# Performance work log

Measured on AMD Instinct MI355X. Metric: run time of the kernel, lower is better.

The kernel has to match this reference:

```python
import jax, jax.numpy as jnp
import numpy as np

N_HEAD = 16
EMBED = 1024
HEAD_DIM = EMBED // N_HEAD  # 64
HALF = HEAD_DIM // 2        # 32
T = 2048                    # total packed tokens
NSEG = 4
SEG = T // NSEG             # 512 tokens per packed sequence
SCALE = HEAD_DIM ** -0.5


def _apply_rotary_vision(t, freqs):
    # t: [T, H, D], freqs: [T, D/2] -> Qwen2-VL style vision RoPE
    cos = jnp.concatenate([jnp.cos(freqs), jnp.cos(freqs)], axis=-1)[:, None, :]  # [T,1,D]
    sin = jnp.concatenate([jnp.sin(freqs), jnp.sin(freqs)], axis=-1)[:, None, :]
    t1, t2 = t[..., :HALF], t[..., HALF:]
    rot = jnp.concatenate([-t2, t1], axis=-1)  # rotate_half
    return t * cos + rot * sin


def setup_inputs() -> dict:
    key = jax.random.key(0)
    k1, k2, k3, k4, k5 = jax.random.split(key, 5)
    hidden_states = jax.random.normal(k1, (T, EMBED), dtype=jnp.float32)
    cu_seqlens = (jnp.arange(NSEG + 1, dtype=jnp.int32) * SEG)  # [0,512,...,2048]
    # realistic rotary freqs: position within each segment * inverse frequencies
    pos = jnp.tile(jnp.arange(SEG, dtype=jnp.float32), NSEG)  # [T]
    inv_freq = 1.0 / (10000.0 ** (jnp.arange(HALF, dtype=jnp.float32) / HALF))
    rotary_pos_emb = pos[:, None] * inv_freq[None, :]  # [T, HALF]
    std = 0.02
    wq = jax.random.normal(k2, (EMBED, EMBED), dtype=jnp.float32) * std
    wk = jax.random.normal(k3, (EMBED, EMBED), dtype=jnp.float32) * std
    wv = jax.random.normal(k4, (EMBED, EMBED), dtype=jnp.float32) * std
    wo = jax.random.normal(k5, (EMBED, EMBED), dtype=jnp.float32) * std
    return {"hidden_states": hidden_states, "cu_seqlens": cu_seqlens,
            "rotary_pos_emb": rotary_pos_emb, "wq": wq, "wk": wk, "wv": wv, "wo": wo}


def reference(hidden_states, cu_seqlens, rotary_pos_emb, wq, wk, wv, wo):
    # QKV projections (nn.Linear, bias=False): y = x @ W.T
    q = (hidden_states @ wq.T).reshape(T, N_HEAD, HEAD_DIM)
    k = (hidden_states @ wk.T).reshape(T, N_HEAD, HEAD_DIM)
    v = (hidden_states @ wv.T).reshape(T, N_HEAD, HEAD_DIM)
    q = _apply_rotary_vision(q, rotary_pos_emb)
    k = _apply_rotary_vision(k, rotary_pos_emb)
    # varlen (block-diagonal, non-causal) attention over packed segments
    seg_id = jnp.searchsorted(cu_seqlens, jnp.arange(T, dtype=cu_seqlens.dtype), side='right')
    same_seg = seg_id[:, None] == seg_id[None, :]  # [T, T]
    scores = jnp.einsum('thd,shd->hts', q, k) * SCALE  # [H, T, T]
    scores = jnp.where(same_seg[None, :, :], scores, jnp.finfo(scores.dtype).min)
    probs = jax.nn.softmax(scores, axis=-1)
    attn = jnp.einsum('hts,shd->thd', probs, v).reshape(T, EMBED)
    return attn @ wo.T
```

## Files before the change

### kernel.cpp

```cpp
#include <hip/hip_runtime.h>
#include <cstdint>

#define T_TOK 2048
#define EMBED 1024
#define NH    16
#define HD    64
#define HALF  32
#define SEG   512
#define SL    (0.125f * 1.44269504088896f)

typedef __attribute__((ext_vector_type(8))) __bf16 bf16x8;
typedef __attribute__((ext_vector_type(4))) float  f32x4;
typedef unsigned short u16;
typedef unsigned int   u32;

__device__ __forceinline__ u16 f2bf(float f) {
  u32 u = __builtin_bit_cast(u32, f);
  u += 0x7fffu + ((u >> 16) & 1u);
  return (u16)(u >> 16);
}

__device__ __forceinline__ void gld_lds16(const void* g, void* l) {
  __builtin_amdgcn_global_load_lds(
      reinterpret_cast<__attribute__((address_space(1))) u32*>(
          reinterpret_cast<uintptr_t>(g)),
      reinterpret_cast<__attribute__((address_space(3))) u32*>(
          reinterpret_cast<uintptr_t>(l)),
      16, 0, 0);
}

__global__ __launch_bounds__(256) void convert_k(
    const float* __restrict__ H,  const float* __restrict__ wq,
    const float* __restrict__ wk, const float* __restrict__ wv,
    const float* __restrict__ wo, u16* __restrict__ dst) {
  const size_t gid = (size_t)blockIdx.x * 256 + threadIdx.x;
  const size_t e = gid * 4;
  const float* src; size_t off;
  const size_t HN = (size_t)T_TOK * EMBED;
  if (e < HN) { src = H; off = e; }
  else {
    size_t r = e - HN;
    int w = (int)(r >> 20);
    off = r & ((1u << 20) - 1);
    src = (w == 0) ? wq : (w == 1) ? wk : (w == 2) ? wv : wo;
  }
  const float4 v = *(const float4*)(src + off);
  ushort4 o;
  o.x = f2bf(v.x); o.y = f2bf(v.y); o.z = f2bf(v.z); o.w = f2bf(v.w);
  *(ushort4*)(dst + e) = o;
}

__global__ __launch_bounds__(256) void qkv_k(
    const u16* __restrict__ Hb, const u16* __restrict__ Wb,
    const float* __restrict__ rope, u16* __restrict__ Qb,
    u16* __restrict__ Khh, u16* __restrict__ Vss) {
  constexpr int K = 1024, N = 1024;
  __shared__ alignas(16) u16 As[2][2][64 * 32];
  __shared__ alignas(16) u16 Bs[2][2][128 * 32];
  const int tid = threadIdx.x;
  const int wave = tid >> 6, lane = tid & 63;
  const int quad = lane >> 4, l16 = lane & 15;
  const int bm = blockIdx.y * 64, bn = blockIdx.x * 128;
  const int z = blockIdx.z;
  const u16* Bz = Wb + ((size_t)z << 20);
  const int wm = (wave >> 1) * 32, wn = (wave & 1) * 64;

  f32x4 acc[2][4];
#pragma unroll
  for (int i = 0; i < 2; ++i)
#pragma unroll
    for (int j = 0; j < 4; ++j) { f32x4 zz = {0.f, 0.f, 0.f, 0.f}; acc[i][j] = zz; }

  const int srow = tid >> 2, scol = (tid & 3) * 8;
  const u16* gA = Hb + (size_t)(bm + srow) * K + scol;
  const u16* gB = Bz + (size_t)(bn + srow) * K + scol;

#pragma unroll
  for (int p = 0; p < 2; ++p) {
    gld_lds16(gA + p * 32, (char*)&As[0][p][0] + wave * 1024);
    gld_lds16(gB + p * 32, (char*)&Bs[0][p][0] + wave * 1024);
    gld_lds16(gB + (size_t)64 * K + p * 32, (char*)&Bs[0][p][64 * 32] + wave * 1024);
  }

  for (int kk = 0; kk < K; kk += 64) {
    __syncthreads();
    const int cur = (kk >> 6) & 1, nxt = cur ^ 1;
    if (kk + 64 < K) {
      const int kn = kk + 64;
#pragma unroll
      for (int p = 0; p < 2; ++p) {
        gld_lds16(gA + kn + p * 32, (char*)&As[nxt][p][0] + wave * 1024);
        gld_lds16(gB + kn + p * 32, (char*)&Bs[nxt][p][0] + wave * 1024);
        gld_lds16(gB + (size_t)64 * K + kn + p * 32,
                  (char*)&Bs[nxt][p][64 * 32] + wave * 1024);
      }
    }
#pragma unroll
    for (int p = 0; p < 2; ++p) {
      const u16* Ac = &As[cur][p][0];
      const u16* Bc = &Bs[cur][p][0];
      bf16x8 af[2], bfv[4];
#pragma unroll
      for (int i = 0; i < 2; ++i)
        af[i] = *(const bf16x8*)(Ac + (wm + i * 16 + l16) * 32 + quad * 8);
#pragma unroll
      for (int j = 0; j < 4; ++j)
        bfv[j] = *(const bf16x8*)(Bc + (wn + j * 16 + l16) * 32 + quad * 8);
#pragma unroll
      for (int i = 0; i < 2; ++i)
#pragma unroll
        for (int j = 0; j < 4; ++j)
          acc[i][j] = __builtin_amdgcn_mfma_f32_16x16x32_bf16(af[i], bfv[j],
                                                              acc[i][j], 0, 0, 0);
    }
  }

  const int h = (bn + wn) >> 6;
  if (z == 0) {
#pragma unroll
    for (int i = 0; i < 2; ++i)
#pragma unroll
      for (int r = 0; r < 4; ++r) {
        const int t = bm + wm + i * 16 + quad * 4 + r;
        const float f0 = rope[t * HALF + l16];
        const float f1 = rope[t * HALF + 16 + l16];
        float s0, c0, s1, c1;
        __sincosf(f0, &s0, &c0);
        __sincosf(f1, &s1, &c1);
        const float v0 = acc[i][0][r], v1 = acc[i][1][r];
        const float v2 = acc[i][2][r], v3 = acc[i][3][r];
        const size_t base = (size_t)t * N + bn + wn + l16;
        Qb[base]      = f2bf(v0 * c0 - v2 * s0);
        Qb[base + 16] = f2bf(v1 * c1 - v3 * s1);
        Qb[base + 32] = f2bf(v2 * c0 + v0 * s0);
        Qb[base + 48] = f2bf(v3 * c1 + v1 * s1);
      }
  } else if (z == 1) {
#pragma unroll
    for (int i = 0; i < 2; ++i)
#pragma unroll
      for (int r = 0; r < 4; ++r) {
        const int t = bm + wm + i * 16 + quad * 4 + r;
        const float f0 = rope[t * HALF + l16];
        const float f1 = rope[t * HALF + 16 + l16];
        float s0, c0, s1, c1;
        __sincosf(f0, &s0, &c0);
        __sincosf(f1, &s1, &c1);
        const float v0 = acc[i][0][r], v1 = acc[i][1][r];
        const float v2 = acc[i][2][r], v3 = acc[i][3][r];
        const size_t b0 = ((size_t)(h * 2 + 0) * T_TOK + t) * 32;
        const size_t b1 = ((size_t)(h * 2 + 1) * T_TOK + t) * 32;
        Khh[b0 + l16]      = f2bf(v0 * c0 - v2 * s0);
        Khh[b0 + 16 + l16] = f2bf(v1 * c1 - v3 * s1);
        Khh[b1 + l16]      = f2bf(v2 * c0 + v0 * s0);
        Khh[b1 + 16 + l16] = f2bf(v3 * c1 + v1 * s1);
      }
  } else {
#pragma unroll
    for (int i = 0; i < 2; ++i) {
      const int t0 = bm + wm + i * 16 + quad * 4;
      const int tp = t0 >> 5, toff = t0 & 31;
#pragma unroll
      for (int j = 0; j < 4; ++j) {
        const int d = j * 16 + l16;
        ushort4 pk;
        pk.x = f2bf(acc[i][j][0]); pk.y = f2bf(acc[i][j][1]);
        pk.z = f2bf(acc[i][j][2]); pk.w = f2bf(acc[i][j][3]);
        *(ushort4*)(Vss + ((size_t)(h * 64 + tp) * 64 + d) * 32 + toff) = pk;
      }
    }
  }
}

__global__ __launch_bounds__(256) void attn_st(
    const u16* __restrict__ Qb, const u16* __restrict__ Khh,
    const u16* __restrict__ Vss, u16* __restrict__ Ab) {
  const int b = blockIdx.x;
  const int qt = b & 7, seg = (b >> 3) & 3, h = b >> 5;
  const int tid = threadIdx.x;
  const int wave = tid >> 6, lane = tid & 63;
  const int quad = lane >> 4, l16 = lane & 15;

  __shared__ alignas(16) u16 Ks[2][64 * 32];
  __shared__ alignas(16) u16 Vs[2][64 * 32];
  __shared__ alignas(16) u16 Pl[4][16 * 72];

  const int qbase = seg * SEG + qt * 64 + wave * 16;
  const u16* qp = Qb + (size_t)(qbase + l16) * EMBED + h * HD + quad * 8;
  const bf16x8 qf0 = *(const bf16x8*)qp;
  const bf16x8 qf1 = *(const bf16x8*)(qp + 32);

  const u16* Ksrc0 = Khh + ((size_t)(h * 2 + 0) * T_TOK + seg * SEG) * 32;
  const u16* Ksrc1 = Khh + ((size_t)(h * 2 + 1) * T_TOK + seg * SEG) * 32;
  const u16* Vsrc  = Vss + ((size_t)(h * 64 + seg * 16) * 64) * 32;

  float mold[4] = {-1e30f, -1e30f, -1e30f, -1e30f};
  float lsum[4] = {0.f, 0.f, 0.f, 0.f};
  f32x4 O[4];
#pragma unroll
  for (int nt = 0; nt < 4; ++nt) { f32x4 z = {0.f, 0.f, 0.f, 0.f}; O[nt] = z; }

  u16* pw = Pl[wave];
  const int toff = tid * 8;

  uint4 kreg0 = *(const uint4*)(Ksrc0 + toff);
  uint4 kreg1 = *(const uint4*)(Ksrc1 + toff);
  uint4 vreg0 = *(const uint4*)(Vsrc + toff);
  uint4 vreg1 = *(const uint4*)(Vsrc + 2048 + toff);

  for (int cc = 0; cc < 8; ++cc) {
    *(uint4*)((char*)&Ks[0][0] + tid * 16) = kreg0;
    *(uint4*)((char*)&Ks[1][0] + tid * 16) = kreg1;
    *(uint4*)((char*)&Vs[0][0] + tid * 16) = vreg0;
    *(uint4*)((char*)&Vs[1][0] + tid * 16) = vreg1;
    __syncthreads();
    if (cc + 1 < 8) {
      const size_t kc = (size_t)(cc + 1) * 2048 + toff;
      const size_t vc = (size_t)(cc + 1) * 4096 + toff;
      kreg0 = *(const uint4*)(Ksrc0 + kc);
      kreg1 = *(const uint4*)(Ksrc1 + kc);
      vreg0 = *(const uint4*)(Vsrc + vc);
      vreg1 = *(const uint4*)(Vsrc + vc + 2048);
    }
    f32x4 S[4];
#pragma unroll
    for (int kt = 0; kt < 4; ++kt) {
      const bf16x8 k0 = *(const bf16x8*)&Ks[0][(kt * 16 + l16) * 32 + quad * 8];
      const bf16x8 k1 = *(const bf16x8*)&Ks[1][(kt * 16 + l16) * 32 + quad * 8];
      f32x4 s = {0.f, 0.f, 0.f, 0.f};
      s = __builtin_amdgcn_mfma_f32_16x16x32_bf16(qf0, k0, s, 0, 0, 0);
      s = __builtin_amdgcn_mfma_f32_16x16x32_bf16(qf1, k1, s, 0, 0, 0);
      S[kt] = s;
    }
    bf16x8 vf0[4], vf1[4];
#pragma unroll
    for (int nt = 0; nt < 4; ++nt) {
      vf0[nt] = *(const bf16x8*)&Vs[0][(nt * 16 + l16) * 32 + quad * 8];
      vf1[nt] = *(const bf16x8*)&Vs[1][(nt * 16 + l16) * 32 + quad * 8];
    }
    float mx[4], al[4];
#pragma unroll
    for (int r = 0; r < 4; ++r) {
      float m = fmaxf(fmaxf(S[0][r], S[1][r]), fmaxf(S[2][r], S[3][r]));
#pragma unroll
      for (int off = 1; off < 16; off <<= 1) m = fmaxf(m, __shfl_xor(m, off));
      float mn = fmaxf(mold[r], m);
      al[r] = exp2f((mold[r] - mn) * SL);
      mold[r] = mn;
      mx[r] = mn;
    }
    float ps[4] = {0.f, 0.f, 0.f, 0.f};
#pragma unroll
    for (int kt = 0; kt < 4; ++kt)
#pragma unroll
      for (int r = 0; r < 4; ++r) {
        float p = exp2f((S[kt][r] - mx[r]) * SL);
        ps[r] += p;
        pw[(quad * 4 + r) * 72 + kt * 16 + l16] = f2bf(p);
      }
#pragma unroll
    for (int r = 0; r < 4; ++r) lsum[r] = lsum[r] * al[r] + ps[r];
#pragma unroll
    for (int nt = 0; nt < 4; ++nt) {
      O[nt][0] *= al[0]; O[nt][1] *= al[1];
      O[nt][2] *= al[2]; O[nt][3] *= al[3];
    }
    const u16* pp = pw + l16 * 72 + quad * 8;
    const bf16x8 pf0 = *(const bf16x8*)pp;
    const bf16x8 pf1 = *(const bf16x8*)(pp + 32);
#pragma unroll
    for (int nt = 0; nt < 4; ++nt) {
      O[nt] = __builtin_amdgcn_mfma_f32_16x16x32_bf16(pf0, vf0[nt], O[nt], 0, 0, 0);
      O[nt] = __builtin_amdgcn_mfma_f32_16x16x32_bf16(pf1, vf1[nt], O[nt], 0, 0, 0);
    }
    __syncthreads();
  }
#pragma unroll
  for (int r = 0; r < 4; ++r) {
    float l = lsum[r];
#pragma unroll
    for (int off = 1; off < 16; off <<= 1) l += __shfl_xor(l, off);
    lsum[r] = 1.f / l;
  }
#pragma unroll
  for (int nt = 0; nt < 4; ++nt)
#pragma unroll
    for (int r = 0; r < 4; ++r) {
      const int trow = qbase + quad * 4 + r;
      Ab[(size_t)trow * EMBED + h * HD + nt * 16 + l16] = f2bf(O[nt][r] * lsum[r]);
    }
}

__global__ __launch_bounds__(256) void oproj_k(
    const u16* __restrict__ Ab, const u16* __restrict__ Wo,
    float* __restrict__ out) {
  constexpr int K = 1024, N = 1024;
  __shared__ alignas(16) u16 As[2][2][64 * 32];
  __shared__ alignas(16) u16 Bs[2][2][64 * 32];
  const int tid = threadIdx.x;
  const int wave = tid >> 6, lane = tid & 63;
  const int quad = lane >> 4, l16 = lane & 15;
  const int bm = blockIdx.y * 64, bn = blockIdx.x * 64;

  f32x4 acc[4];
#pragma unroll
  for (int j = 0; j < 4; ++j) { f32x4 z = {0.f, 0.f, 0.f, 0.f}; acc[j] = z; }

  const int srow = tid >> 2, scol = (tid & 3) * 8;
  const u16* gA = Ab + (size_t)(bm + srow) * K + scol;
  const u16* gB = Wo + (size_t)(bn + srow) * K + scol;

#pragma unroll
  for (int p = 0; p < 2; ++p) {
    gld_lds16(gA + p * 32, (char*)&As[0][p][0] + wave * 1024);
    gld_lds16(gB + p * 32, (char*)&Bs[0][p][0] + wave * 1024);
  }

  for (int kk = 0; kk < K; kk += 64) {
    __syncthreads();
    const int cur = (kk >> 6) & 1, nxt = cur ^ 1;
    if (kk + 64 < K) {
      const int kn = kk + 64;
#pragma unroll
      for (int p = 0; p < 2; ++p) {
        gld_lds16(gA + kn + p * 32, (char*)&As[nxt][p][0] + wave * 1024);
        gld_lds16(gB + kn + p * 32, (char*)&Bs[nxt][p][0] + wave * 1024);
      }
    }
#pragma unroll
    for (int p = 0; p < 2; ++p) {
      const u16* Ac = &As[cur][p][0];
      const u16* Bc = &Bs[cur][p][0];
      const bf16x8 af = *(const bf16x8*)(Ac + (wave * 16 + l16) * 32 + quad * 8);
      bf16x8 bfv[4];
#pragma unroll
      for (int j = 0; j < 4; ++j)
        bfv[j] = *(const bf16x8*)(Bc + (j * 16 + l16) * 32 + quad * 8);
#pragma unroll
      for (int j = 0; j < 4; ++j)
        acc[j] = __builtin_amdgcn_mfma_f32_16x16x32_bf16(af, bfv[j],
                                                         acc[j], 0, 0, 0);
    }
  }

#pragma unroll
  for (int r = 0; r < 4; ++r) {
    const int row = bm + wave * 16 + quad * 4 + r;
#pragma unroll
    for (int j = 0; j < 4; ++j)
      out[(size_t)row * N + bn + j * 16 + l16] = acc[j][r];
  }
}

extern "C" void kernel_launch(void* const* d_in, const int* in_sizes, int n_in,
                              void* d_out, int out_size, void* d_ws,
                              size_t ws_size, hipStream_t stream) {
  const float* H    = (const float*)d_in[0];
  const float* rope = (const float*)d_in[2];
  const float* wq   = (const float*)d_in[3];
  const float* wk   = (const float*)d_in[4];
  const float* wv   = (const float*)d_in[5];
  const float* wo   = (const float*)d_in[6];
  float* out        = (float*)d_out;

  constexpr size_t M1 = (size_t)1 << 20;
  if (ws_size < 28 * M1) return;

  u16* ws16 = (u16*)d_ws;
  u16* Hb  = ws16;
  u16* Wb  = ws16 + 2 * M1;
  u16* Qb  = ws16 + 6 * M1;
  u16* Khh = ws16 + 8 * M1;
  u16* Vss = ws16 + 10 * M1;
  u16* Ab  = ws16 + 12 * M1;

  convert_k<<<6144, 256, 0, stream>>>(H, wq, wk, wv, wo, ws16);
  qkv_k<<<dim3(8, 32, 3), 256, 0, stream>>>(Hb, Wb, rope, Qb, Khh, Vss);
  attn_st<<<512, 256, 0, stream>>>(Qb, Khh, Vss, Ab);
  oproj_k<<<dim3(16, 32), 256, 0, stream>>>(Ab, Wb + 3 * M1, out);
}
```

Before: 131.6 us.

## Pre-pack GEMM operands into MFMA fragment layout and load directly to registers

The conversion kernel now writes hidden states and weights in a tiled layout where each 16x32 MFMA fragment is contiguous, and attention writes its output in the same packed layout. The QKV and output-projection GEMMs then drop LDS staging and barriers, reading fragments straight from global memory into registers with a two-stage register double buffer. This removes LDS traffic and __syncthreads, but gives up the sharing of tiles across waves that LDS provided, so each wave reloads operands from global/L2.

```diff
diff --git a/kernel.cpp b/kernel.cpp
--- a/kernel.cpp
+++ b/kernel.cpp
@@ -20,13 +20,9 @@
   return (u16)(u >> 16);
 }
 
-__device__ __forceinline__ void gld_lds16(const void* g, void* l) {
-  __builtin_amdgcn_global_load_lds(
-      reinterpret_cast<__attribute__((address_space(1))) u32*>(
-          reinterpret_cast<uintptr_t>(g)),
-      reinterpret_cast<__attribute__((address_space(3))) u32*>(
-          reinterpret_cast<uintptr_t>(l)),
-      16, 0, 0);
+__device__ __forceinline__ size_t pidx(int t, int k) {
+  return ((size_t)((t >> 4) * 32 + (k >> 5)) << 9) +
+         ((((k >> 3) & 3) * 16 + (t & 15)) << 3) + (k & 7);
 }
 
 __global__ __launch_bounds__(256) void convert_k(
@@ -34,36 +30,42 @@
     const float* __restrict__ wk, const float* __restrict__ wv,
     const float* __restrict__ wo, u16* __restrict__ dst) {
   const size_t gid = (size_t)blockIdx.x * 256 + threadIdx.x;
-  const size_t e = gid * 4;
-  const float* src; size_t off;
+  const size_t e8 = gid * 8;
+  const float* src; size_t off, base;
   const size_t HN = (size_t)T_TOK * EMBED;
-  if (e < HN) { src = H; off = e; }
+  if (e8 < HN) { src = H; off = e8; base = 0; }
   else {
-    size_t r = e - HN;
+    size_t r = e8 - HN;
     int w = (int)(r >> 20);
     off = r & ((1u << 20) - 1);
     src = (w == 0) ? wq : (w == 1) ? wk : (w == 2) ? wv : wo;
-  }
-  const float4 v = *(const float4*)(src + off);
-  ushort4 o;
-  o.x = f2bf(v.x); o.y = f2bf(v.y); o.z = f2bf(v.z); o.w = f2bf(v.w);
-  *(ushort4*)(dst + e) = o;
+    base = HN + ((size_t)w << 20);
+  }
+  const int t = (int)(off >> 10), k = (int)(off & 1023);
+  const float4 v0 = *(const float4*)(src + off);
+  const float4 v1 = *(const float4*)(src + off + 4);
+  ushort4 o0, o1;
+  o0.x = f2bf(v0.x); o0.y = f2bf(v0.y); o0.z = f2bf(v0.z); o0.w = f2bf(v0.w);
+  o1.x = f2bf(v1.x); o1.y = f2bf(v1.y); o1.z = f2bf(v1.z); o1.w = f2bf(v1.w);
+  u16* d = dst + base + pidx(t, k);
+  *(ushort4*)d = o0;
+  *(ushort4*)(d + 4) = o1;
 }
 
 __global__ __launch_bounds__(256) void qkv_k(
-    const u16* __restrict__ Hb, const u16* __restrict__ Wb,
+    const u16* __restrict__ Hp, const u16* __restrict__ Wp,
     const float* __restrict__ rope, u16* __restrict__ Qb,
     u16* __restrict__ Khh, u16* __restrict__ Vss) {
-  constexpr int K = 1024, N = 1024;
-  __shared__ alignas(16) u16 As[2][2][64 * 32];
-  __shared__ alignas(16) u16 Bs[2][2][128 * 32];
+  constexpr int N = 1024;
   const int tid = threadIdx.x;
   const int wave = tid >> 6, lane = tid & 63;
   const int quad = lane >> 4, l16 = lane & 15;
   const int bm = blockIdx.y * 64, bn = blockIdx.x * 128;
   const int z = blockIdx.z;
-  const u16* Bz = Wb + ((size_t)z << 20);
+  const u16* Bp = Wp + ((size_t)z << 20);
   const int wm = (wave >> 1) * 32, wn = (wave & 1) * 64;
+  const int t16 = (bm + wm) >> 4;
+  const int n16 = (bn + wn) >> 4;
 
   f32x4 acc[2][4];
 #pragma unroll
@@ -71,47 +73,48 @@
 #pragma unroll
     for (int j = 0; j < 4; ++j) { f32x4 zz = {0.f, 0.f, 0.f, 0.f}; acc[i][j] = zz; }
 
-  const int srow = tid >> 2, scol = (tid & 3) * 8;
-  const u16* gA = Hb + (size_t)(bm + srow) * K + scol;
-  const u16* gB = Bz + (size_t)(bn + srow) * K + scol;
-
-#pragma unroll
-  for (int p = 0; p < 2; ++p) {
-    gld_lds16(gA + p * 32, (char*)&As[0][p][0] + wave * 1024);
-    gld_lds16(gB + p * 32, (char*)&Bs[0][p][0] + wave * 1024);
-    gld_lds16(gB + (size_t)64 * K + p * 32, (char*)&Bs[0][p][64 * 32] + wave * 1024);
-  }
-
-  for (int kk = 0; kk < K; kk += 64) {
-    __syncthreads();
-    const int cur = (kk >> 6) & 1, nxt = cur ^ 1;
-    if (kk + 64 < K) {
-      const int kn = kk + 64;
-#pragma unroll
-      for (int p = 0; p < 2; ++p) {
-        gld_lds16(gA + kn + p * 32, (char*)&As[nxt][p][0] + wave * 1024);
-        gld_lds16(gB + kn + p * 32, (char*)&Bs[nxt][p][0] + wave * 1024);
-        gld_lds16(gB + (size_t)64 * K + kn + p * 32,
-                  (char*)&Bs[nxt][p][64 * 32] + wave * 1024);
-      }
-    }
-#pragma unroll
-    for (int p = 0; p < 2; ++p) {
-      const u16* Ac = &As[cur][p][0];
-      const u16* Bc = &Bs[cur][p][0];
-      bf16x8 af[2], bfv[4];
+  const u16* pa = Hp + ((size_t)t16 << 14) + lane * 8;
+  const u16* pb = Bp + ((size_t)n16 << 14) + lane * 8;
+
+  bf16x8 aF[2][2], bF[2][4];
+#pragma unroll
+  for (int s = 0; s < 2; ++s) {
+#pragma unroll
+    for (int i = 0; i < 2; ++i)
+      aF[s][i] = *(const bf16x8*)(pa + (((size_t)i * 32 + s) << 9));
+#pragma unroll
+    for (int j = 0; j < 4; ++j)
+      bF[s][j] = *(const bf16x8*)(pb + (((size_t)j * 32 + s) << 9));
+  }
+
+  for (int kp = 0; kp < 32; kp += 2) {
+#pragma unroll
+    for (int i = 0; i < 2; ++i)
+#pragma unroll
+      for (int j = 0; j < 4; ++j)
+        acc[i][j] = __builtin_amdgcn_mfma_f32_16x16x32_bf16(aF[0][i], bF[0][j],
+                                                            acc[i][j], 0, 0, 0);
+    if (kp + 2 < 32) {
 #pragma unroll
       for (int i = 0; i < 2; ++i)
-        af[i] = *(const bf16x8*)(Ac + (wm + i * 16 + l16) * 32 + quad * 8);
-#pragma unroll
-      for (int j = 0; j < 4; ++j)
-        bfv[j] = *(const bf16x8*)(Bc + (wn + j * 16 + l16) * 32 + quad * 8);
+        aF[0][i] = *(const bf16x8*)(pa + (((size_t)i * 32 + kp + 2) << 9));
+#pragma unroll
+      for (int j = 0; j < 4; ++j)
+        bF[0][j] = *(const bf16x8*)(pb + (((size_t)j * 32 + kp + 2) << 9));
+    }
+#pragma unroll
+    for (int i = 0; i < 2; ++i)
+#pragma unroll
+      for (int j = 0; j < 4; ++j)
+        acc[i][j] = __builtin_amdgcn_mfma_f32_16x16x32_bf16(aF[1][i], bF[1][j],
+                                                            acc[i][j], 0, 0, 0);
+    if (kp + 3 < 32) {
 #pragma unroll
       for (int i = 0; i < 2; ++i)
-#pragma unroll
-        for (int j = 0; j < 4; ++j)
-          acc[i][j] = __builtin_amdgcn_mfma_f32_16x16x32_bf16(af[i], bfv[j],
-                                                              acc[i][j], 0, 0, 0);
+        aF[1][i] = *(const bf16x8*)(pa + (((size_t)i * 32 + kp + 3) << 9));
+#pragma unroll
+      for (int j = 0; j < 4; ++j)
+        bF[1][j] = *(const bf16x8*)(pb + (((size_t)j * 32 + kp + 3) << 9));
     }
   }
 
@@ -174,7 +177,7 @@
 
 __global__ __launch_bounds__(256) void attn_st(
     const u16* __restrict__ Qb, const u16* __restrict__ Khh,
-    const u16* __restrict__ Vss, u16* __restrict__ Ab) {
+    const u16* __restrict__ Vss, u16* __restrict__ Abp) {
   const int b = blockIdx.x;
   const int qt = b & 7, seg = (b >> 3) & 3, h = b >> 5;
   const int tid = threadIdx.x;
@@ -282,64 +285,65 @@
     for (int off = 1; off < 16; off <<= 1) l += __shfl_xor(l, off);
     lsum[r] = 1.f / l;
   }
-#pragma unroll
-  for (int nt = 0; nt < 4; ++nt)
-#pragma unroll
-    for (int r = 0; r < 4; ++r) {
-      const int trow = qbase + quad * 4 + r;
-      Ab[(size_t)trow * EMBED + h * HD + nt * 16 + l16] = f2bf(O[nt][r] * lsum[r]);
-    }
+  const int t16 = qbase >> 4;
+#pragma unroll
+  for (int nt = 0; nt < 4; ++nt) {
+    const int kp = h * 2 + (nt >> 1);
+    const int k32q = (nt & 1) * 2 + (l16 >> 3);
+    u16* dst = Abp + (((size_t)t16 * 32 + kp) << 9) + (l16 & 7);
+#pragma unroll
+    for (int r = 0; r < 4; ++r)
+      dst[(size_t)(k32q * 16 + quad * 4 + r) << 3] = f2bf(O[nt][r] * lsum[r]);
+  }
 }
 
 __global__ __launch_bounds__(256) void oproj_k(
-    const u16* __restrict__ Ab, const u16* __restrict__ Wo,
+    const u16* __restrict__ Abp, const u16* __restrict__ Wop,
     float* __restrict__ out) {
-  constexpr int K = 1024, N = 1024;
-  __shared__ alignas(16) u16 As[2][2][64 * 32];
-  __shared__ alignas(16) u16 Bs[2][2][64 * 32];
+  constexpr int N = 1024;
   const int tid = threadIdx.x;
   const int wave = tid >> 6, lane = tid & 63;
   const int quad = lane >> 4, l16 = lane & 15;
   const int bm = blockIdx.y * 64, bn = blockIdx.x * 64;
+  const int t16 = (bm + wave * 16) >> 4;
+  const int n16 = bn >> 4;
 
   f32x4 acc[4];
 #pragma unroll
   for (int j = 0; j < 4; ++j) { f32x4 z = {0.f, 0.f, 0.f, 0.f}; acc[j] = z; }
 
-  const int srow = tid >> 2, scol = (tid & 3) * 8;
-  const u16* gA = Ab + (size_t)(bm + srow) * K + scol;
-  const u16* gB = Wo + (size_t)(bn + srow) * K + scol;
-
-#pragma unroll
-  for (int p = 0; p < 2; ++p) {
-    gld_lds16(gA + p * 32, (char*)&As[0][p][0] + wave * 1024);
-    gld_lds16(gB + p * 32, (char*)&Bs[0][p][0] + wave * 1024);
-  }
-
-  for (int kk = 0; kk < K; kk += 64) {
-    __syncthreads();
-    const int cur = (kk >> 6) & 1, nxt = cur ^ 1;
-    if (kk + 64 < K) {
-      const int kn = kk + 64;
-#pragma unroll
-      for (int p = 0; p < 2; ++p) {
-        gld_lds16(gA + kn + p * 32, (char*)&As[nxt][p][0] + wave * 1024);
-        gld_lds16(gB + kn + p * 32, (char*)&Bs[nxt][p][0] + wave * 1024);
-      }
-    }
-#pragma unroll
-    for (int p = 0; p < 2; ++p) {
-      const u16* Ac = &As[cur][p][0];
-      const u16* Bc = &Bs[cur][p][0];
-      const bf16x8 af = *(const bf16x8*)(Ac + (wave * 16 + l16) * 32 + quad * 8);
-      bf16x8 bfv[4];
-#pragma unroll
-      for (int j = 0; j < 4; ++j)
-        bfv[j] = *(const bf16x8*)(Bc + (j * 16 + l16) * 32 + quad * 8);
-#pragma unroll
-      for (int j = 0; j < 4; ++j)
-        acc[j] = __builtin_amdgcn_mfma_f32_16x16x32_bf16(af, bfv[j],
-                                                         acc[j], 0, 0, 0);
+  const u16* pa = Abp + ((size_t)t16 << 14) + lane * 8;
+  const u16* pb = Wop + ((size_t)n16 << 14) + lane * 8;
+
+  bf16x8 aF[2], bF[2][4];
+#pragma unroll
+  for (int s = 0; s < 2; ++s) {
+    aF[s] = *(const bf16x8*)(pa + ((size_t)s << 9));
+#pragma unroll
+    for (int j = 0; j < 4; ++j)
+      bF[s][j] = *(const bf16x8*)(pb + (((size_t)j * 32 + s) << 9));
+  }
+
+  for (int kp = 0; kp < 32; kp += 2) {
+#pragma unroll
+    for (int j = 0; j < 4; ++j)
+      acc[j] = __builtin_amdgcn_mfma_f32_16x16x32_bf16(aF[0], bF[0][j],
+                                                       acc[j], 0, 0, 0);
+    if (kp + 2 < 32) {
+      aF[0] = *(const bf16x8*)(pa + ((size_t)(kp + 2) << 9));
+#pragma unroll
+      for (int j = 0; j < 4; ++j)
+        bF[0][j] = *(const bf16x8*)(pb + (((size_t)j * 32 + kp + 2) << 9));
+    }
+#pragma unroll
+    for (int j = 0; j < 4; ++j)
+      acc[j] = __builtin_amdgcn_mfma_f32_16x16x32_bf16(aF[1], bF[1][j],
+                                                       acc[j], 0, 0, 0);
+    if (kp + 3 < 32) {
+      aF[1] = *(const bf16x8*)(pa + ((size_t)(kp + 3) << 9));
+#pragma unroll
+      for (int j = 0; j < 4; ++j)
+        bF[1][j] = *(const bf16x8*)(pb + (((size_t)j * 32 + kp + 3) << 9));
     }
   }
 
@@ -367,15 +371,15 @@
   if (ws_size < 28 * M1) return;
 
   u16* ws16 = (u16*)d_ws;
-  u16* Hb  = ws16;
-  u16* Wb  = ws16 + 2 * M1;
+  u16* Hp  = ws16;
+  u16* Wp  = ws16 + 2 * M1;
   u16* Qb  = ws16 + 6 * M1;
   u16* Khh = ws16 + 8 * M1;
   u16* Vss = ws16 + 10 * M1;
-  u16* Ab  = ws16 + 12 * M1;
-
-  convert_k<<<6144, 256, 0, stream>>>(H, wq, wk, wv, wo, ws16);
-  qkv_k<<<dim3(8, 32, 3), 256, 0, stream>>>(Hb, Wb, rope, Qb, Khh, Vss);
-  attn_st<<<512, 256, 0, stream>>>(Qb, Khh, Vss, Ab);
-  oproj_k<<<dim3(16, 32), 256, 0, stream>>>(Ab, Wb + 3 * M1, out);
-}
+  u16* Abp = ws16 + 12 * M1;
+
+  convert_k<<<3072, 256, 0, stream>>>(H, wq, wk, wv, wo, ws16);
+  qkv_k<<<dim3(8, 32, 3), 256, 0, stream>>>(Hp, Wp, rope, Qb, Khh, Vss);
+  attn_st<<<512, 256, 0, stream>>>(Qb, Khh, Vss, Abp);
+  oproj_k<<<dim3(16, 32), 256, 0, stream>>>(Abp, Wp + 3 * M1, out);
+}
```

After: 144.0 us. 9.5% more time.
